# Kernel tuning notes

Measured on AMD Instinct MI355X. Metric: run time of the kernel, lower is better.

The kernel has to match this reference:

```python
import jax, jax.numpy as jnp
import numpy as np

EMBED_DIM = 384
HEAD_SIZE = 64
BLOCK = 256
BATCH = 256

def setup_inputs() -> dict:
    key = jax.random.key(0)
    k1, k2, k3, k4 = jax.random.split(key, 4)
    x = jax.random.normal(k1, (BATCH, BLOCK, EMBED_DIM), dtype=jnp.float32)
    # nn.Linear-style init scale (not exact torch init, just reasonable magnitude)
    s = 1.0 / np.sqrt(EMBED_DIM)
    Wq = jax.random.normal(k2, (EMBED_DIM, HEAD_SIZE), dtype=jnp.float32) * s
    Wk = jax.random.normal(k3, (EMBED_DIM, HEAD_SIZE), dtype=jnp.float32) * s
    Wv = jax.random.normal(k4, (EMBED_DIM, HEAD_SIZE), dtype=jnp.float32) * s
    return {"x": x, "Wq": Wq, "Wk": Wk, "Wv": Wv}

def reference(x, Wq, Wk, Wv):
    # single-head causal self-attention (dropout in eval mode => identity)
    b, t, _ = x.shape
    q = jnp.einsum('btc,ch->bth', x, Wq)          # [B,T,H]
    k = jnp.einsum('btc,ch->bth', x, Wk)
    v = jnp.einsum('btc,ch->bth', x, Wv)
    scale = k.shape[-1] ** -0.5
    wei = jnp.einsum('bth,bsh->bts', q, k) * scale  # [B,T,T]
    causal = jnp.tril(jnp.ones((t, t), dtype=bool))
    wei = jnp.where(causal, wei, -jnp.inf)
    wei = jax.nn.softmax(wei, axis=-1)
    return jnp.einsum('bts,bsh->bth', wei, v)      # [B,T,H]
```

## Files before the change

### kernel.cpp

```cpp
#include <hip/hip_runtime.h>


#define B_ 256
#define T_ 256
#define C_ 384
#define H_ 64

typedef __attribute__((ext_vector_type(4))) float     f32x4;
typedef __attribute__((ext_vector_type(8))) _Float16  f16x8;

#define MFMA16(a, b, c) __builtin_amdgcn_mfma_f32_16x16x32_f16((a), (b), (c), 0, 0, 0)
#define LGKM_BARRIER() do { asm volatile("s_waitcnt lgkmcnt(0)" ::: "memory"); \
                            __builtin_amdgcn_s_barrier(); } while (0)

constexpr int SQ = 72;
constexpr int SV = 264;
constexpr int SP = 72;
constexpr int OFF_V  = 256 * SQ;
constexpr int OFF_R3 = OFF_V + 64 * SV;
constexpr int OFF_WS = OFF_R3 + 256 * SQ;
constexpr int SMEM_HALFS = OFF_WS + 24 * 512;
constexpr int SMEM_BYTES = SMEM_HALFS * 2;

__global__ void w_fragpack(const float* __restrict__ Wq,
                           const float* __restrict__ Wk,
                           const float* __restrict__ Wv,
                           _Float16* __restrict__ Wf) {
    int e = blockIdx.x * 256 + threadIdx.x;
    int i    = e & 7;
    int lane = (e >> 3) & 63;
    int l15  = lane & 15, hi = lane >> 4;
    int cid  = e >> 9;
    int kk   = cid % 12;
    int nt   = cid / 12;
    int col  = nt * 16 + l15;
    int p    = col >> 6;
    int h    = col & 63;
    int k    = kk * 32 + hi * 8 + i;
    const float* W = (p == 0) ? Wq : (p == 1) ? Wk : Wv;
    Wf[e] = (_Float16)W[k * 64 + h];
}

__device__ __forceinline__ void issue_chunk(const float* xb, const _Float16* Wf,
    int tid, int c, float4 (&xu)[8], f16x8 (&w)[3])
{
    #pragma unroll
    for (int i = 0; i < 4; ++i) {
        int id = tid + i * 512, row = id >> 3, g = id & 7;
        const float* gp = xb + row * C_ + c * 64 + g * 8;
        xu[2 * i]     = *(const float4*)gp;
        xu[2 * i + 1] = *(const float4*)(gp + 4);
    }
    #pragma unroll
    for (int i = 0; i < 3; ++i) {
        int s = tid + i * 512, f = s >> 6, ls = s & 63;
        int nt = f >> 1, kc2 = f & 1;
        w[i] = *(const f16x8*)(Wf + ((size_t)((nt * 12 + 2 * c + kc2) * 64) + ls) * 8);
    }
}

__device__ __forceinline__ void write_chunk(_Float16* XB, _Float16* WS,
    int tid, const float4 (&xu)[8], const f16x8 (&w)[3])
{
    #pragma unroll
    for (int i = 0; i < 4; ++i) {
        int id = tid + i * 512, row = id >> 3, g = id & 7;
        const float4& a = xu[2 * i];
        const float4& b = xu[2 * i + 1];
        f16x8 hv = {(_Float16)a.x, (_Float16)a.y, (_Float16)a.z, (_Float16)a.w,
                    (_Float16)b.x, (_Float16)b.y, (_Float16)b.z, (_Float16)b.w};
        *(f16x8*)(XB + row * SQ + g * 8) = hv;
    }
    #pragma unroll
    for (int i = 0; i < 3; ++i) {
        int s = tid + i * 512;
        *(f16x8*)(WS + s * 8) = w[i];
    }
}

__global__ __launch_bounds__(512, 1) void head_fused(
    const float* __restrict__ x, const _Float16* __restrict__ Wf,
    float* __restrict__ out)
{
    extern __shared__ _Float16 sm[];
    _Float16* Ks = sm;
    _Float16* Vt = sm + OFF_V;
    _Float16* XB = sm + OFF_R3;
    _Float16* WS = sm + OFF_WS;
    _Float16* Qs = sm + OFF_R3;
    _Float16* Ps = sm + OFF_R3;

    const int tid = threadIdx.x, lane = tid & 63, wid = tid >> 6;
    const int lo = lane & 15, hi = lane >> 4;
    const int b = blockIdx.x;
    const float* xb = x + (size_t)b * T_ * C_;

    float4 xA[8], xB2[8];
    f16x8  wA[3], wB[3];
    issue_chunk(xb, Wf, tid, 0, xA, wA);
    issue_chunk(xb, Wf, tid, 1, xB2, wB);
    write_chunk(XB, WS, tid, xA, wA);
    LGKM_BARRIER();

    f32x4 acc[12][2] = {};
    #pragma unroll
    for (int c = 0; c < 6; ++c) {
        if (c + 2 < 6) {
            if ((c & 1) == 0) issue_chunk(xb, Wf, tid, c + 2, xA, wA);
            else              issue_chunk(xb, Wf, tid, c + 2, xB2, wB);
        }

        #pragma unroll
        for (int kc2 = 0; kc2 < 2; ++kc2) {
            f16x8 a0 = *(const f16x8*)(XB + (32 * wid + lo) * SQ + kc2 * 32 + hi * 8);
            f16x8 a1 = *(const f16x8*)(XB + (32 * wid + 16 + lo) * SQ + kc2 * 32 + hi * 8);
            #pragma unroll
            for (int nt = 0; nt < 8; ++nt) {
                f16x8 wf = *(const f16x8*)(WS + ((nt * 2 + kc2) * 64 + lane) * 8);
                acc[nt][0] = MFMA16(a0, wf, acc[nt][0]);
                acc[nt][1] = MFMA16(a1, wf, acc[nt][1]);
            }
            #pragma unroll
            for (int nt = 8; nt < 12; ++nt) {
                f16x8 wf = *(const f16x8*)(WS + ((nt * 2 + kc2) * 64 + lane) * 8);
                acc[nt][0] = MFMA16(wf, a0, acc[nt][0]);
                acc[nt][1] = MFMA16(wf, a1, acc[nt][1]);
            }
        }

        if (c < 5) {
            LGKM_BARRIER();
            if ((c & 1) == 0) write_chunk(XB, WS, tid, xB2, wB);
            else              write_chunk(XB, WS, tid, xA, wA);
            LGKM_BARRIER();
        }
    }

    #pragma unroll
    for (int nt = 0; nt < 4; ++nt)
        #pragma unroll
        for (int s = 0; s < 2; ++s)
            #pragma unroll
            for (int reg = 0; reg < 4; ++reg) {
                int t = 32 * wid + s * 16 + 4 * hi + reg;
                Qs[t * SQ + nt * 16 + lo] = (_Float16)(0.125f * acc[nt][s][reg]);
            }
    #pragma unroll
    for (int nt = 4; nt < 8; ++nt)
        #pragma unroll
        for (int s = 0; s < 2; ++s)
            #pragma unroll
            for (int reg = 0; reg < 4; ++reg) {
                int t = 32 * wid + s * 16 + 4 * hi + reg;
                Ks[t * SQ + (nt - 4) * 16 + lo] = (_Float16)acc[nt][s][reg];
            }
    #pragma unroll
    for (int nt = 8; nt < 12; ++nt)
        #pragma unroll
        for (int s = 0; s < 2; ++s)
            #pragma unroll
            for (int reg = 0; reg < 4; ++reg) {
                int h = (nt - 8) * 16 + 4 * hi + reg;
                int t = 32 * wid + s * 16 + lo;
                Vt[h * SV + t] = (_Float16)acc[nt][s][reg];
            }
    LGKM_BARRIER();

    const int ctmax = 2 * wid + 1;

    f16x8 aq[2][2];
    #pragma unroll
    for (int rt = 0; rt < 2; ++rt)
        #pragma unroll
        for (int ks = 0; ks < 2; ++ks)
            aq[rt][ks] = *(const f16x8*)(Qs + (32 * wid + 16 * rt + lo) * SQ + 32 * ks + 8 * hi);

    f32x4 sacc[2][16] = {};
    #pragma unroll
    for (int ct = 0; ct < 16; ++ct) {
        if (ct <= ctmax) {
            #pragma unroll
            for (int ks = 0; ks < 2; ++ks) {
                f16x8 bk = *(const f16x8*)(Ks + (16 * ct + lo) * SQ + 32 * ks + 8 * hi);
                sacc[0][ct] = MFMA16(aq[0][ks], bk, sacc[0][ct]);
                sacc[1][ct] = MFMA16(aq[1][ks], bk, sacc[1][ct]);
            }
        }
    }

    #pragma unroll
    for (int rt = 0; rt < 2; ++rt) {
        #pragma unroll
        for (int reg = 0; reg < 4; ++reg) {
            const int rowg = 32 * wid + 16 * rt + 4 * hi + reg;
            float m = -1e30f;
            #pragma unroll
            for (int ct = 0; ct < 16; ++ct) if (ct <= ctmax) {
                float v = sacc[rt][ct][reg];
                v = (16 * ct + lo <= rowg) ? v : -1e30f;
                sacc[rt][ct][reg] = v;
                m = fmaxf(m, v);
            }
            #pragma unroll
            for (int s = 1; s < 16; s <<= 1) m = fmaxf(m, __shfl_xor(m, s, 16));
            float l = 0.f;
            #pragma unroll
            for (int ct = 0; ct < 16; ++ct) if (ct <= ctmax) {
                float v = sacc[rt][ct][reg];
                float p = (v > -1e29f) ? __expf(v - m) : 0.f;
                sacc[rt][ct][reg] = p;
                l += p;
            }
            #pragma unroll
            for (int s = 1; s < 16; s <<= 1) l += __shfl_xor(l, s, 16);
            float rinv = 1.f / l;
            #pragma unroll
            for (int ct = 0; ct < 16; ++ct) if (ct <= ctmax) sacc[rt][ct][reg] *= rinv;
        }
    }

    f32x4 oacc[2][4] = {};
    _Float16* Pw = Ps + wid * 32 * SP;
    const int kcmax = ctmax >> 2;
    #pragma unroll
    for (int kc = 0; kc < 4; ++kc) {
        if (kc <= kcmax) {
            #pragma unroll
            for (int rt = 0; rt < 2; ++rt)
                #pragma unroll
                for (int cc = 0; cc < 4; ++cc) {
                    const int ct = 4 * kc + cc;
                    #pragma unroll
                    for (int reg = 0; reg < 4; ++reg) {
                        float v = (ct <= ctmax) ? sacc[rt][ct][reg] : 0.f;
                        Pw[(16 * rt + 4 * hi + reg) * SP + cc * 16 + lo] = (_Float16)v;
                    }
                }
            asm volatile("s_waitcnt lgkmcnt(0)" ::: "memory");
            #pragma unroll
            for (int ks = 0; ks < 2; ++ks) {
                f16x8 p0 = *(const f16x8*)(Pw + lo * SP + 32 * ks + 8 * hi);
                f16x8 p1 = *(const f16x8*)(Pw + (16 + lo) * SP + 32 * ks + 8 * hi);
                #pragma unroll
                for (int ht = 0; ht < 4; ++ht) {
                    f16x8 bv = *(const f16x8*)(Vt + (16 * ht + lo) * SV + 64 * kc + 32 * ks + 8 * hi);
                    oacc[0][ht] = MFMA16(p0, bv, oacc[0][ht]);
                    oacc[1][ht] = MFMA16(p1, bv, oacc[1][ht]);
                }
            }
            asm volatile("s_waitcnt lgkmcnt(0)" ::: "memory");
        }
    }

    float* ob = out + (size_t)b * (T_ * H_);
    #pragma unroll
    for (int rt = 0; rt < 2; ++rt)
        #pragma unroll
        for (int ht = 0; ht < 4; ++ht)
            #pragma unroll
            for (int reg = 0; reg < 4; ++reg) {
                const int t = 32 * wid + 16 * rt + 4 * hi + reg;
                ob[t * H_ + 16 * ht + lo] = oacc[rt][ht][reg];
            }
}

extern "C" void kernel_launch(void* const* d_in, const int* in_sizes, int n_in,
                              void* d_out, int out_size, void* d_ws, size_t ws_size,
                              hipStream_t stream) {
    const float* x  = (const float*)d_in[0];
    const float* Wq = (const float*)d_in[1];
    const float* Wk = (const float*)d_in[2];
    const float* Wv = (const float*)d_in[3];
    float* out = (float*)d_out;
    (void)in_sizes; (void)n_in; (void)out_size; (void)ws_size;

    _Float16* Wf = (_Float16*)d_ws;

    w_fragpack<<<dim3(288), dim3(256), 0, stream>>>(Wq, Wk, Wv, Wf);
    hipFuncSetAttribute(reinterpret_cast<const void*>(head_fused),
                        hipFuncAttributeMaxDynamicSharedMemorySize, SMEM_BYTES);
    head_fused<<<dim3(B_), dim3(512), SMEM_BYTES, stream>>>(x, Wf, out);
}
```

Baseline: 42.58 us.

## Use 1024 threads per block with 16 rows per wave

Doubles the workgroup from 8 to 16 waves, so each wave owns one 16-row tile instead of two in the projection, score, softmax and PV stages. Loads and the register tile shapes are adjusted to match. The goal is more waves per CU to hide latency and spread the causal work across more waves. In exchange, each B fragment is reused by only one MFMA instead of two, the LDS traffic per MFMA for weight and K/V fragments goes up, and the launch-bounds register budget is tighter.

```diff
diff --git a/kernel.cpp b/kernel.cpp
--- a/kernel.cpp
+++ b/kernel.cpp
@@ -42,29 +42,32 @@
 }
 
 __device__ __forceinline__ void issue_chunk(const float* xb, const _Float16* Wf,
-    int tid, int c, float4 (&xu)[8], f16x8 (&w)[3])
+    int tid, int c, float4 (&xu)[4], f16x8 (&w)[2])
 {
     #pragma unroll
-    for (int i = 0; i < 4; ++i) {
-        int id = tid + i * 512, row = id >> 3, g = id & 7;
+    for (int i = 0; i < 2; ++i) {
+        int id = tid + i * 1024, row = id >> 3, g = id & 7;
         const float* gp = xb + row * C_ + c * 64 + g * 8;
         xu[2 * i]     = *(const float4*)gp;
         xu[2 * i + 1] = *(const float4*)(gp + 4);
     }
     #pragma unroll
-    for (int i = 0; i < 3; ++i) {
-        int s = tid + i * 512, f = s >> 6, ls = s & 63;
-        int nt = f >> 1, kc2 = f & 1;
-        w[i] = *(const f16x8*)(Wf + ((size_t)((nt * 12 + 2 * c + kc2) * 64) + ls) * 8);
+    for (int i = 0; i < 2; ++i) {
+        int s = tid + i * 1024;
+        if (s < 1536) {
+            int f = s >> 6, ls = s & 63;
+            int nt = f >> 1, kc2 = f & 1;
+            w[i] = *(const f16x8*)(Wf + ((size_t)((nt * 12 + 2 * c + kc2) * 64) + ls) * 8);
+        }
     }
 }
 
 __device__ __forceinline__ void write_chunk(_Float16* XB, _Float16* WS,
-    int tid, const float4 (&xu)[8], const f16x8 (&w)[3])
+    int tid, const float4 (&xu)[4], const f16x8 (&w)[2])
 {
     #pragma unroll
-    for (int i = 0; i < 4; ++i) {
-        int id = tid + i * 512, row = id >> 3, g = id & 7;
+    for (int i = 0; i < 2; ++i) {
+        int id = tid + i * 1024, row = id >> 3, g = id & 7;
         const float4& a = xu[2 * i];
         const float4& b = xu[2 * i + 1];
         f16x8 hv = {(_Float16)a.x, (_Float16)a.y, (_Float16)a.z, (_Float16)a.w,
@@ -72,13 +75,13 @@
         *(f16x8*)(XB + row * SQ + g * 8) = hv;
     }
     #pragma unroll
-    for (int i = 0; i < 3; ++i) {
-        int s = tid + i * 512;
-        *(f16x8*)(WS + s * 8) = w[i];
-    }
-}
-
-__global__ __launch_bounds__(512, 1) void head_fused(
+    for (int i = 0; i < 2; ++i) {
+        int s = tid + i * 1024;
+        if (s < 1536) *(f16x8*)(WS + s * 8) = w[i];
+    }
+}
+
+__global__ __launch_bounds__(1024, 4) void head_fused(
     const float* __restrict__ x, const _Float16* __restrict__ Wf,
     float* __restrict__ out)
 {
@@ -95,14 +98,14 @@
     const int b = blockIdx.x;
     const float* xb = x + (size_t)b * T_ * C_;
 
-    float4 xA[8], xB2[8];
-    f16x8  wA[3], wB[3];
+    float4 xA[4], xB2[4];
+    f16x8  wA[2], wB[2];
     issue_chunk(xb, Wf, tid, 0, xA, wA);
     issue_chunk(xb, Wf, tid, 1, xB2, wB);
     write_chunk(XB, WS, tid, xA, wA);
     LGKM_BARRIER();
 
-    f32x4 acc[12][2] = {};
+    f32x4 acc[12] = {};
     #pragma unroll
     for (int c = 0; c < 6; ++c) {
         if (c + 2 < 6) {
@@ -112,19 +115,16 @@
 
         #pragma unroll
         for (int kc2 = 0; kc2 < 2; ++kc2) {
-            f16x8 a0 = *(const f16x8*)(XB + (32 * wid + lo) * SQ + kc2 * 32 + hi * 8);
-            f16x8 a1 = *(const f16x8*)(XB + (32 * wid + 16 + lo) * SQ + kc2 * 32 + hi * 8);
+            f16x8 a0 = *(const f16x8*)(XB + (16 * wid + lo) * SQ + kc2 * 32 + hi * 8);
             #pragma unroll
             for (int nt = 0; nt < 8; ++nt) {
                 f16x8 wf = *(const f16x8*)(WS + ((nt * 2 + kc2) * 64 + lane) * 8);
-                acc[nt][0] = MFMA16(a0, wf, acc[nt][0]);
-                acc[nt][1] = MFMA16(a1, wf, acc[nt][1]);
+                acc[nt] = MFMA16(a0, wf, acc[nt]);
             }
             #pragma unroll
             for (int nt = 8; nt < 12; ++nt) {
                 f16x8 wf = *(const f16x8*)(WS + ((nt * 2 + kc2) * 64 + lane) * 8);
-                acc[nt][0] = MFMA16(wf, a0, acc[nt][0]);
-                acc[nt][1] = MFMA16(wf, a1, acc[nt][1]);
+                acc[nt] = MFMA16(wf, a0, acc[nt]);
             }
         }
 
@@ -139,113 +139,97 @@
     #pragma unroll
     for (int nt = 0; nt < 4; ++nt)
         #pragma unroll
-        for (int s = 0; s < 2; ++s)
-            #pragma unroll
-            for (int reg = 0; reg < 4; ++reg) {
-                int t = 32 * wid + s * 16 + 4 * hi + reg;
-                Qs[t * SQ + nt * 16 + lo] = (_Float16)(0.125f * acc[nt][s][reg]);
-            }
+        for (int reg = 0; reg < 4; ++reg) {
+            int t = 16 * wid + 4 * hi + reg;
+            Qs[t * SQ + nt * 16 + lo] = (_Float16)(0.125f * acc[nt][reg]);
+        }
     #pragma unroll
     for (int nt = 4; nt < 8; ++nt)
         #pragma unroll
-        for (int s = 0; s < 2; ++s)
-            #pragma unroll
-            for (int reg = 0; reg < 4; ++reg) {
-                int t = 32 * wid + s * 16 + 4 * hi + reg;
-                Ks[t * SQ + (nt - 4) * 16 + lo] = (_Float16)acc[nt][s][reg];
-            }
+        for (int reg = 0; reg < 4; ++reg) {
+            int t = 16 * wid + 4 * hi + reg;
+            Ks[t * SQ + (nt - 4) * 16 + lo] = (_Float16)acc[nt][reg];
+        }
     #pragma unroll
     for (int nt = 8; nt < 12; ++nt)
         #pragma unroll
-        for (int s = 0; s < 2; ++s)
-            #pragma unroll
-            for (int reg = 0; reg < 4; ++reg) {
-                int h = (nt - 8) * 16 + 4 * hi + reg;
-                int t = 32 * wid + s * 16 + lo;
-                Vt[h * SV + t] = (_Float16)acc[nt][s][reg];
-            }
+        for (int reg = 0; reg < 4; ++reg) {
+            int h = (nt - 8) * 16 + 4 * hi + reg;
+            int t = 16 * wid + lo;
+            Vt[h * SV + t] = (_Float16)acc[nt][reg];
+        }
     LGKM_BARRIER();
 
-    const int ctmax = 2 * wid + 1;
-
-    f16x8 aq[2][2];
-    #pragma unroll
-    for (int rt = 0; rt < 2; ++rt)
-        #pragma unroll
-        for (int ks = 0; ks < 2; ++ks)
-            aq[rt][ks] = *(const f16x8*)(Qs + (32 * wid + 16 * rt + lo) * SQ + 32 * ks + 8 * hi);
-
-    f32x4 sacc[2][16] = {};
+    const int ctmax = wid;
+
+    f16x8 aq[2];
+    #pragma unroll
+    for (int ks = 0; ks < 2; ++ks)
+        aq[ks] = *(const f16x8*)(Qs + (16 * wid + lo) * SQ + 32 * ks + 8 * hi);
+
+    f32x4 sacc[16] = {};
     #pragma unroll
     for (int ct = 0; ct < 16; ++ct) {
         if (ct <= ctmax) {
             #pragma unroll
             for (int ks = 0; ks < 2; ++ks) {
                 f16x8 bk = *(const f16x8*)(Ks + (16 * ct + lo) * SQ + 32 * ks + 8 * hi);
-                sacc[0][ct] = MFMA16(aq[0][ks], bk, sacc[0][ct]);
-                sacc[1][ct] = MFMA16(aq[1][ks], bk, sacc[1][ct]);
-            }
-        }
-    }
-
-    #pragma unroll
-    for (int rt = 0; rt < 2; ++rt) {
-        #pragma unroll
-        for (int reg = 0; reg < 4; ++reg) {
-            const int rowg = 32 * wid + 16 * rt + 4 * hi + reg;
-            float m = -1e30f;
-            #pragma unroll
-            for (int ct = 0; ct < 16; ++ct) if (ct <= ctmax) {
-                float v = sacc[rt][ct][reg];
-                v = (16 * ct + lo <= rowg) ? v : -1e30f;
-                sacc[rt][ct][reg] = v;
-                m = fmaxf(m, v);
-            }
-            #pragma unroll
-            for (int s = 1; s < 16; s <<= 1) m = fmaxf(m, __shfl_xor(m, s, 16));
-            float l = 0.f;
-            #pragma unroll
-            for (int ct = 0; ct < 16; ++ct) if (ct <= ctmax) {
-                float v = sacc[rt][ct][reg];
-                float p = (v > -1e29f) ? __expf(v - m) : 0.f;
-                sacc[rt][ct][reg] = p;
-                l += p;
-            }
-            #pragma unroll
-            for (int s = 1; s < 16; s <<= 1) l += __shfl_xor(l, s, 16);
-            float rinv = 1.f / l;
-            #pragma unroll
-            for (int ct = 0; ct < 16; ++ct) if (ct <= ctmax) sacc[rt][ct][reg] *= rinv;
-        }
-    }
-
-    f32x4 oacc[2][4] = {};
-    _Float16* Pw = Ps + wid * 32 * SP;
+                sacc[ct] = MFMA16(aq[ks], bk, sacc[ct]);
+            }
+        }
+    }
+
+    #pragma unroll
+    for (int reg = 0; reg < 4; ++reg) {
+        const int rowg = 16 * wid + 4 * hi + reg;
+        float m = -1e30f;
+        #pragma unroll
+        for (int ct = 0; ct < 16; ++ct) if (ct <= ctmax) {
+            float v = sacc[ct][reg];
+            v = (16 * ct + lo <= rowg) ? v : -1e30f;
+            sacc[ct][reg] = v;
+            m = fmaxf(m, v);
+        }
+        #pragma unroll
+        for (int s = 1; s < 16; s <<= 1) m = fmaxf(m, __shfl_xor(m, s, 16));
+        float l = 0.f;
+        #pragma unroll
+        for (int ct = 0; ct < 16; ++ct) if (ct <= ctmax) {
+            float v = sacc[ct][reg];
+            float p = (v > -1e29f) ? __expf(v - m) : 0.f;
+            sacc[ct][reg] = p;
+            l += p;
+        }
+        #pragma unroll
+        for (int s = 1; s < 16; s <<= 1) l += __shfl_xor(l, s, 16);
+        float rinv = 1.f / l;
+        #pragma unroll
+        for (int ct = 0; ct < 16; ++ct) if (ct <= ctmax) sacc[ct][reg] *= rinv;
+    }
+
+    f32x4 oacc[4] = {};
+    _Float16* Pw = Ps + wid * 16 * SP;
     const int kcmax = ctmax >> 2;
     #pragma unroll
     for (int kc = 0; kc < 4; ++kc) {
         if (kc <= kcmax) {
             #pragma unroll
-            for (int rt = 0; rt < 2; ++rt)
+            for (int cc = 0; cc < 4; ++cc) {
+                const int ct = 4 * kc + cc;
                 #pragma unroll
-                for (int cc = 0; cc < 4; ++cc) {
-                    const int ct = 4 * kc + cc;
-                    #pragma unroll
-                    for (int reg = 0; reg < 4; ++reg) {
-                        float v = (ct <= ctmax) ? sacc[rt][ct][reg] : 0.f;
-                        Pw[(16 * rt + 4 * hi + reg) * SP + cc * 16 + lo] = (_Float16)v;
-                    }
+                for (int reg = 0; reg < 4; ++reg) {
+                    float v = (ct <= ctmax) ? sacc[ct][reg] : 0.f;
+                    Pw[(4 * hi + reg) * SP + cc * 16 + lo] = (_Float16)v;
                 }
+            }
             asm volatile("s_waitcnt lgkmcnt(0)" ::: "memory");
             #pragma unroll
             for (int ks = 0; ks < 2; ++ks) {
                 f16x8 p0 = *(const f16x8*)(Pw + lo * SP + 32 * ks + 8 * hi);
-                f16x8 p1 = *(const f16x8*)(Pw + (16 + lo) * SP + 32 * ks + 8 * hi);
                 #pragma unroll
                 for (int ht = 0; ht < 4; ++ht) {
                     f16x8 bv = *(const f16x8*)(Vt + (16 * ht + lo) * SV + 64 * kc + 32 * ks + 8 * hi);
-                    oacc[0][ht] = MFMA16(p0, bv, oacc[0][ht]);
-                    oacc[1][ht] = MFMA16(p1, bv, oacc[1][ht]);
+                    oacc[ht] = MFMA16(p0, bv, oacc[ht]);
                 }
             }
             asm volatile("s_waitcnt lgkmcnt(0)" ::: "memory");
@@ -254,14 +238,12 @@
 
     float* ob = out + (size_t)b * (T_ * H_);
     #pragma unroll
-    for (int rt = 0; rt < 2; ++rt)
-        #pragma unroll
-        for (int ht = 0; ht < 4; ++ht)
-            #pragma unroll
-            for (int reg = 0; reg < 4; ++reg) {
-                const int t = 32 * wid + 16 * rt + 4 * hi + reg;
-                ob[t * H_ + 16 * ht + lo] = oacc[rt][ht][reg];
-            }
+    for (int ht = 0; ht < 4; ++ht)
+        #pragma unroll
+        for (int reg = 0; reg < 4; ++reg) {
+            const int t = 16 * wid + 4 * hi + reg;
+            ob[t * H_ + 16 * ht + lo] = oacc[ht][reg];
+        }
 }
 
 extern "C" void kernel_launch(void* const* d_in, const int* in_sizes, int n_in,
@@ -279,5 +261,5 @@
     w_fragpack<<<dim3(288), dim3(256), 0, stream>>>(Wq, Wk, Wv, Wf);
     hipFuncSetAttribute(reinterpret_cast<const void*>(head_fused),
                         hipFuncAttributeMaxDynamicSharedMemorySize, SMEM_BYTES);
-    head_fused<<<dim3(B_), dim3(512), SMEM_BYTES, stream>>>(x, Wf, out);
-}
+    head_fused<<<dim3(B_), dim3(1024), SMEM_BYTES, stream>>>(x, Wf, out);
+}
```

Result: slower. 49.57 us (+16.4%).
